# Kernel optimization log

Measured on AMD Instinct MI355X. Metric: run time of the kernel, lower is better.

The kernel has to match this reference:

```python
import jax, jax.numpy as jnp
import numpy as np

NUM_SCOPE = 64
NUM_SAMPLE = 16
DIM_ENCODE = 64


def _fixed_basis(dim):
    # FixedTimeEncoder / FixedFrequencyEncoder basis: w_i = 1 / 10^(9*i/(dim-1))
    return (1.0 / 10.0 ** jnp.linspace(0.0, 9.0, dim)).astype(jnp.float32)


def _cos_encode(t, dim):
    # t: [...] -> [..., dim]
    w = _fixed_basis(dim)
    return jnp.cos(t[..., None] * w)


def setup_inputs() -> dict:
    key = jax.random.key(0)
    ks = jax.random.split(key, 12)
    n, b, df = 4096, NUM_SCOPE, 172
    s_in = 1.0 / np.sqrt(df)
    return {
        "root_node_feature": jax.random.normal(ks[0], (n, df), jnp.float32),
        "root_ts": jax.random.uniform(ks[1], (n,), jnp.float32) * 1e4,
        "neighbor_node_feature": jax.random.normal(ks[2], (n, b, df), jnp.float32),
        "neighbor_edge_feature": jax.random.normal(ks[3], (n, b, df), jnp.float32),
        "neighbor_ts": jax.random.uniform(ks[4], (n, b), jnp.float32) * 1e4,
        "neighbor_nid": jax.random.randint(ks[5], (n, b), 0, 10000, jnp.int64) if jax.config.jax_enable_x64 else jax.random.randint(ks[5], (n, b), 0, 10000, jnp.int32),
        "W_node": jax.random.normal(ks[6], (df, 64), jnp.float32) * s_in,
        "b_node": jnp.zeros((64,), jnp.float32),
        "W_edge": jax.random.normal(ks[7], (df, 64), jnp.float32) * s_in,
        "b_edge": jnp.zeros((64,), jnp.float32),
        "W_link": jax.random.normal(ks[8], (320, 256), jnp.float32) / np.sqrt(320),
        "W_root": jax.random.normal(ks[9], (192, 256), jnp.float32) / np.sqrt(192),
    }


def reference(root_node_feature, root_ts, neighbor_node_feature,
              neighbor_edge_feature, neighbor_ts, neighbor_nid,
              W_node, b_node, W_edge, b_edge, W_link, W_root):
    n, b = neighbor_nid.shape
    # --- encode root node ---
    root_feat = jax.nn.relu(root_node_feature @ W_node + b_node)          # [n,64]
    root_time = _cos_encode(jnp.zeros((n,), jnp.float32), DIM_ENCODE)     # [n,64]
    root_freq = _cos_encode(jnp.ones((n,), jnp.float32), DIM_ENCODE)      # [n,64]
    root_encode = jnp.concatenate([root_feat, root_time, root_freq], 1)   # [n,192]
    # --- encode links ---
    node_enc = jax.nn.relu(neighbor_node_feature @ W_node + b_node)       # [n,b,64]
    edge_enc = jax.nn.relu(neighbor_edge_feature @ W_edge + b_edge)       # [n,b,64]
    neigh_time = root_ts[:, None] - neighbor_ts                           # [n,b]
    time_enc = _cos_encode(neigh_time, DIM_ENCODE)                        # [n,b,64]
    # pairwise equality mask + frequency count (keep_dummy_freq=True)
    neigh_mask = (neighbor_nid[:, :, None] == neighbor_nid[:, None, :])   # [n,b,b]
    neigh_freq = neigh_mask.sum(-1).astype(jnp.float32) / NUM_SCOPE       # [n,b]
    freq_enc = _cos_encode(neigh_freq, DIM_ENCODE)                        # [n,b,64]
    iden_enc = neigh_mask.astype(jnp.float32)                             # [n,b,b]
    link_encode = jnp.concatenate(
        [node_enc, edge_enc, time_enc, freq_enc, iden_enc], axis=-1)      # [n,b,320]
    # --- link mapper: project links & root, score, softmax over neighbors ---
    h_link = jax.nn.relu(jnp.einsum('nbd,dh->nbh', link_encode, W_link))  # [n,b,256]
    h_root = jax.nn.relu(root_encode @ W_root)                            # [n,256]
    scores = jnp.einsum('nbh,nh->nb', h_link, h_root) / jnp.sqrt(256.0)
    probs = jax.nn.softmax(scores, axis=-1)                               # [n,b]
    # --- weighted sampling WITHOUT replacement via Gumbel top-k ---
    g = jax.random.gumbel(jax.random.key(42), (n, b), jnp.float32)
    logp = jnp.log(probs + 1e-20)
    _, action = jax.lax.top_k(logp + g, NUM_SAMPLE)                       # [n,num_sample]
    return probs, action
```

## Files before the change

kernel.cpp:

```cpp
#include <hip/hip_runtime.h>
#include <cstdint>
#include <math.h>

#define B       64
#define DF      172
#define HDIM    256
#define KSAMP   16
#define THREADS 512

typedef const __attribute__((address_space(1))) unsigned int* gp_t;
typedef __attribute__((address_space(3))) unsigned int* lp_t;

#define FMA4(A_, S_, W_) \
  A_.x = fmaf(S_, W_.x, A_.x); A_.y = fmaf(S_, W_.y, A_.y); \
  A_.z = fmaf(S_, W_.z, A_.z); A_.w = fmaf(S_, W_.w, A_.w);

__device__ __forceinline__ uint32_t rotl32(uint32_t x, int d) {
  return (x << d) | (x >> (32 - d));
}

__device__ __forceinline__ void threefry2x32(uint32_t k0, uint32_t k1,
                                             uint32_t& x0, uint32_t& x1) {
  const uint32_t ks0 = k0, ks1 = k1, ks2 = k0 ^ k1 ^ 0x1BD11BDAu;
  x0 += ks0; x1 += ks1;
#define TF_R4(ra,rb,rc,rd) \
  x0 += x1; x1 = rotl32(x1, ra); x1 ^= x0; \
  x0 += x1; x1 = rotl32(x1, rb); x1 ^= x0; \
  x0 += x1; x1 = rotl32(x1, rc); x1 ^= x0; \
  x0 += x1; x1 = rotl32(x1, rd); x1 ^= x0;
  TF_R4(13,15,26,6)  x0 += ks1; x1 += ks2 + 1u;
  TF_R4(17,29,16,24) x0 += ks2; x1 += ks0 + 2u;
  TF_R4(13,15,26,6)  x0 += ks0; x1 += ks1 + 3u;
  TF_R4(17,29,16,24) x0 += ks1; x1 += ks2 + 4u;
  TF_R4(13,15,26,6)  x0 += ks2; x1 += ks0 + 5u;
#undef TF_R4
}

__device__ __forceinline__ void stage_async(const float* __restrict__ g,
                                            float* l, int t) {
#pragma unroll
  for (int it = 0; it < 5; ++it) {
    const int i  = it * 512 + t;
    const int ib = it * 512 + (t & ~63);
    __builtin_amdgcn_global_load_lds((gp_t)(g + i * 4), (lp_t)(l + ib * 4), 16, 0, 0);
  }
  if (t < 192) {
    const int i  = 2560 + t;
    const int ib = 2560 + (t & ~63);
    __builtin_amdgcn_global_load_lds((gp_t)(g + i * 4), (lp_t)(l + ib * 4), 16, 0, 0);
  }
}

#define ENC_STEP(W0_, W1_, W2_, W3_, KK_) { \
  const float4 x0 = A0[(KK_) >> 2]; \
  const float4 x1 = A1[(KK_) >> 2]; \
  FMA4(acc0, x0.x, W0_) FMA4(acc0, x0.y, W1_) FMA4(acc0, x0.z, W2_) FMA4(acc0, x0.w, W3_) \
  FMA4(acc1, x1.x, W0_) FMA4(acc1, x1.y, W1_) FMA4(acc1, x1.z, W2_) FMA4(acc1, x1.w, W3_) }

#define ENC_LOAD(W0_, W1_, W2_, W3_, KK_) { \
  W0_ = W4[(KK_) * 16 + cg]; W1_ = W4[((KK_) + 1) * 16 + cg]; \
  W2_ = W4[((KK_) + 2) * 16 + cg]; W3_ = W4[((KK_) + 3) * 16 + cg]; }

__device__ __forceinline__ void enc_gemm_ring(const float* __restrict__ stage,
                                              const float* __restrict__ W,
                                              const float* __restrict__ bias,
                                              float* __restrict__ out,
                                              int b2, int cg) {
  const float4* W4 = (const float4*)W;
  const float4* A0 = (const float4*)(stage + (2 * b2) * DF);
  const float4* A1 = (const float4*)(stage + (2 * b2 + 1) * DF);
  float4 acc0 = ((const float4*)bias)[cg];
  float4 acc1 = acc0;
  float4 a0, a1, a2, a3, b0, b1, b2_, b3, c0, c1, c2, c3;
  ENC_LOAD(a0, a1, a2, a3, 0)
  ENC_LOAD(b0, b1, b2_, b3, 4)
  ENC_LOAD(c0, c1, c2, c3, 8)
  for (int k0 = 0; k0 < 156; k0 += 12) {
    ENC_STEP(a0, a1, a2, a3, k0)       ENC_LOAD(a0, a1, a2, a3, k0 + 12)
    ENC_STEP(b0, b1, b2_, b3, k0 + 4)  ENC_LOAD(b0, b1, b2_, b3, k0 + 16)
    ENC_STEP(c0, c1, c2, c3, k0 + 8)   ENC_LOAD(c0, c1, c2, c3, k0 + 20)
  }
  ENC_STEP(a0, a1, a2, a3, 156)  ENC_LOAD(a0, a1, a2, a3, 168)
  ENC_STEP(b0, b1, b2_, b3, 160)
  ENC_STEP(c0, c1, c2, c3, 164)
  ENC_STEP(a0, a1, a2, a3, 168)
  float4 o0 = make_float4(fmaxf(acc0.x, 0.f), fmaxf(acc0.y, 0.f), fmaxf(acc0.z, 0.f), fmaxf(acc0.w, 0.f));
  float4 o1 = make_float4(fmaxf(acc1.x, 0.f), fmaxf(acc1.y, 0.f), fmaxf(acc1.z, 0.f), fmaxf(acc1.w, 0.f));
  ((float4*)out)[(2 * b2) * 16 + cg]     = o0;
  ((float4*)out)[(2 * b2 + 1) * 16 + cg] = o1;
}

__device__ __forceinline__ void enc_gemm_lite(const float* __restrict__ stage,
                                              const float* __restrict__ W,
                                              const float* __restrict__ bias,
                                              float* __restrict__ out,
                                              int b2, int cg) {
  const float4* W4 = (const float4*)W;
  const float4* A0 = (const float4*)(stage + (2 * b2) * DF);
  const float4* A1 = (const float4*)(stage + (2 * b2 + 1) * DF);
  float4 acc0 = ((const float4*)bias)[cg];
  float4 acc1 = acc0;
  float4 w0 = W4[0 * 16 + cg], w1 = W4[1 * 16 + cg];
  float4 w2 = W4[2 * 16 + cg], w3 = W4[3 * 16 + cg];
  for (int k = 0; k < DF; k += 4) {
    const float4 wa = w0, wb = w1, wc = w2, wd = w3;
    if (k < DF - 4) {
      w0 = W4[(k + 4) * 16 + cg]; w1 = W4[(k + 5) * 16 + cg];
      w2 = W4[(k + 6) * 16 + cg]; w3 = W4[(k + 7) * 16 + cg];
    }
    ENC_STEP(wa, wb, wc, wd, k)
  }
  float4 o0 = make_float4(fmaxf(acc0.x, 0.f), fmaxf(acc0.y, 0.f), fmaxf(acc0.z, 0.f), fmaxf(acc0.w, 0.f));
  float4 o1 = make_float4(fmaxf(acc1.x, 0.f), fmaxf(acc1.y, 0.f), fmaxf(acc1.z, 0.f), fmaxf(acc1.w, 0.f));
  ((float4*)out)[(2 * b2) * 16 + cg]     = o0;
  ((float4*)out)[(2 * b2 + 1) * 16 + cg] = o1;
}

__device__ __forceinline__ void accum16(float2 (&acc)[16],
                                        const float* __restrict__ enc, int r16,
                                        const float2* __restrict__ Wlp) {
  float2 w0 = Wlp[0], w1 = Wlp[128], w2 = Wlp[256], w3 = Wlp[384];
  for (int d0 = 0; d0 < 64; d0 += 4) {
    const float2 wa = w0, wb = w1, wc = w2, wd = w3;
    if (d0 < 60) {
      const float2* p = Wlp + (d0 + 4) * 128;
      w0 = p[0]; w1 = p[128]; w2 = p[256]; w3 = p[384];
    }
#pragma unroll
    for (int i = 0; i < 16; ++i) {
      const float4 e = *(const float4*)&enc[(r16 + i) * 64 + d0];
      acc[i].x = fmaf(e.x, wa.x, acc[i].x); acc[i].y = fmaf(e.x, wa.y, acc[i].y);
      acc[i].x = fmaf(e.y, wb.x, acc[i].x); acc[i].y = fmaf(e.y, wb.y, acc[i].y);
      acc[i].x = fmaf(e.z, wc.x, acc[i].x); acc[i].y = fmaf(e.z, wc.y, acc[i].y);
      acc[i].x = fmaf(e.w, wd.x, acc[i].x); acc[i].y = fmaf(e.w, wd.y, acc[i].y);
    }
  }
}

__global__ __launch_bounds__(THREADS, 4)
void AdaptSampler_kernel(const float* __restrict__ rootf,
                         const float* __restrict__ root_ts,
                         const float* __restrict__ nf,
                         const float* __restrict__ ef,
                         const float* __restrict__ nts,
                         const int*   __restrict__ nid,
                         const float* __restrict__ Wn,
                         const float* __restrict__ bn,
                         const float* __restrict__ We,
                         const float* __restrict__ be,
                         const float* __restrict__ Wl,
                         const float* __restrict__ Wr,
                         float* __restrict__ out_probs,
                         float* __restrict__ out_action)
{
  __shared__ float nf_stage[B * DF];
  __shared__ float encA[B * 64];
  __shared__ float encB[B * 64];
  __shared__ float hroot_lds[HDIM];
  __shared__ float rootenc_lds[192];
  __shared__ float w_lds[B];
  __shared__ float ts_lds[B];
  __shared__ __align__(16) int nid_lds[B];
  __shared__ float freq_lds[B];
  __shared__ unsigned long long mask_lds[B];
  __shared__ float scpart[4][16][2];

  const int n = blockIdx.x;
  const int t = threadIdx.x;
  const int c2  = t & 127;
  const int r16 = (t >> 7) * 16;
  const int b2 = t >> 4;
  const int cg = t & 15;
  const float2* Wl2 = (const float2*)Wl;

  stage_async(nf + (size_t)n * B * DF, nf_stage, t);
  if (t >= 448) {
    const int j = t - 448;
    double e = 9.0 * (double)j / 63.0;
    const float wj = (float)(1.0 / pow(10.0, e));
    w_lds[j]   = wj;
    nid_lds[j] = nid[n * B + j];
    ts_lds[j]  = nts[n * B + j];
    float a = bn[j];
    const float* rr = rootf + (size_t)n * DF;
#pragma unroll 4
    for (int d = 0; d < DF; ++d) a = fmaf(rr[d], Wn[d * 64 + j], a);
    rootenc_lds[j]       = fmaxf(a, 0.0f);
    rootenc_lds[64 + j]  = 1.0f;
    rootenc_lds[128 + j] = cosf(wj);
    const int my = nid_lds[j];
    unsigned long long m = 0ull;
    for (int k = 0; k < B; ++k)
      m |= ((unsigned long long)(nid_lds[k] == my)) << k;
    mask_lds[j] = m;
    freq_lds[j] = (float)__popcll(m) * 0.015625f;
  }
  __syncthreads();

  enc_gemm_ring(nf_stage, Wn, bn, encA, b2, cg);
  {
    const float rts = root_ts[n];
#pragma unroll
    for (int q = 0; q < 8; ++q) {
      const int idx = q * 512 + t;
      const int bb = idx >> 6, dd = idx & 63;
      encB[idx] = cosf((rts - ts_lds[bb]) * w_lds[dd]);
    }
  }
  {
    const int h = t >> 1, hf = t & 1;
    float a = 0.0f;
    for (int d = hf * 96; d < hf * 96 + 96; ++d)
      a = fmaf(rootenc_lds[d], Wr[d * HDIM + h], a);
    a += __shfl_xor(a, 1);
    if (hf == 0) hroot_lds[h] = fmaxf(a, 0.0f);
  }
  __syncthreads();

  stage_async(ef + (size_t)n * B * DF, nf_stage, t);
  float2 acc[16];
#pragma unroll
  for (int i = 0; i < 16; ++i) acc[i] = make_float2(0.f, 0.f);
  accum16(acc, encA, r16, Wl2 + c2);
  __syncthreads();

  enc_gemm_lite(nf_stage, We, be, encA, b2, cg);
  __syncthreads();

#pragma unroll
  for (int q = 0; q < 8; ++q) {
    const int idx = q * 512 + t;
    const int bb = idx >> 6, dd = idx & 63;
    nf_stage[idx] = cosf(freq_lds[bb] * w_lds[dd]);
  }
  accum16(acc, encA, r16, Wl2 + 64 * 128 + c2);
  __syncthreads();

  accum16(acc, encB, r16, Wl2 + 128 * 128 + c2);
  accum16(acc, nf_stage, r16, Wl2 + 192 * 128 + c2);
  {
    const float2* Wlp = Wl2 + 256 * 128 + c2;
#pragma unroll
    for (int i = 0; i < 16; ++i) {
      unsigned long long m = mask_lds[r16 + i];
      while (m) {
        const int d = __builtin_ctzll(m);
        m &= m - 1;
        const float2 wv = Wlp[d * 128];
        acc[i].x += wv.x;
        acc[i].y += wv.y;
      }
    }
  }

  {
    const float2 hr = ((const float2*)hroot_lds)[c2];
#pragma unroll
    for (int i = 0; i < 16; ++i) {
      float s = fmaxf(acc[i].x, 0.f) * hr.x;
      s = fmaf(fmaxf(acc[i].y, 0.f), hr.y, s);
#pragma unroll
      for (int mm = 32; mm >= 1; mm >>= 1) s += __shfl_xor(s, mm);
      if ((t & 63) == 0) scpart[t >> 7][i][(t >> 6) & 1] = s;
    }
  }
  __syncthreads();

  if (t < B) {
    float s = (scpart[t >> 4][t & 15][0] + scpart[t >> 4][t & 15][1]) * 0.0625f;
    float m = s;
#pragma unroll
    for (int mm = 32; mm >= 1; mm >>= 1) m = fmaxf(m, __shfl_xor(m, mm));
    float e = expf(s - m);
    float sum = e;
#pragma unroll
    for (int mm = 32; mm >= 1; mm >>= 1) sum += __shfl_xor(sum, mm);
    float p = e / sum;
    out_probs[(size_t)n * B + t] = p;

    uint32_t i = (uint32_t)(n * B + t);
    uint32_t x0 = 0u, x1 = i;
    threefry2x32(0u, 42u, x0, x1);
    uint32_t bits = x0 ^ x1;
    float f = __uint_as_float((bits >> 9) | 0x3f800000u) - 1.0f;
    const float TINY = 1.1754943508222875e-38f;
    float u = fmaxf(f * (1.0f - TINY) + TINY, TINY);
    float g = -logf(-logf(u));
    float keyv = logf(p + 1e-20f) + g;

    float v = keyv;
    for (int k = 0; k < KSAMP; ++k) {
      float bv = v; int bi = t;
#pragma unroll
      for (int mm = 32; mm >= 1; mm >>= 1) {
        float ov = __shfl_xor(bv, mm);
        int   oi = __shfl_xor(bi, mm);
        if (ov > bv || (ov == bv && oi < bi)) { bv = ov; bi = oi; }
      }
      if (t == 0) out_action[(size_t)n * KSAMP + k] = (float)bi;
      if (t == bi) v = -3.402823466e+38f;
    }
  }
}

extern "C" void kernel_launch(void* const* d_in, const int* in_sizes, int n_in,
                              void* d_out, int out_size, void* d_ws, size_t ws_size,
                              hipStream_t stream) {
  const float* rootf = (const float*)d_in[0];
  const float* rts   = (const float*)d_in[1];
  const float* nf    = (const float*)d_in[2];
  const float* ef    = (const float*)d_in[3];
  const float* nts   = (const float*)d_in[4];
  const int*   nid   = (const int*)d_in[5];
  const float* Wn    = (const float*)d_in[6];
  const float* bn    = (const float*)d_in[7];
  const float* We    = (const float*)d_in[8];
  const float* be    = (const float*)d_in[9];
  const float* Wl    = (const float*)d_in[10];
  const float* Wr    = (const float*)d_in[11];

  const int n = in_sizes[1];
  float* probs  = (float*)d_out;
  float* action = probs + (size_t)n * B;

  AdaptSampler_kernel<<<dim3(n), dim3(THREADS), 0, stream>>>(
      rootf, rts, nf, ef, nts, nid, Wn, bn, We, be, Wl, Wr, probs, action);
}
```

Baseline: 879.3 us.

## Split each row's neighbors across two blocks and move softmax/top-k to second kernel

The fused per-row kernel is split in two. The first runs a 2D grid where each 256-thread block handles half of a row's 64 neighbors (32 each) and writes raw scores. A second small kernel then does the softmax, Gumbel noise and top-k per row. This halves per-block LDS so more blocks can be resident and parallelism rises. The cost is a second launch, a global round-trip for the scores, and duplicated root-encoding and h_root work in both half-blocks.

```diff
diff --git a/kernel.cpp b/kernel.cpp
--- a/kernel.cpp
+++ b/kernel.cpp
@@ -3,10 +3,11 @@
 #include <math.h>
 
 #define B       64
+#define RH      32
 #define DF      172
 #define HDIM    256
 #define KSAMP   16
-#define THREADS 512
+#define T1      256
 
 typedef const __attribute__((address_space(1))) unsigned int* gp_t;
 typedef __attribute__((address_space(3))) unsigned int* lp_t;
@@ -36,17 +37,17 @@
 #undef TF_R4
 }
 
-__device__ __forceinline__ void stage_async(const float* __restrict__ g,
-                                            float* l, int t) {
+__device__ __forceinline__ void stage32(const float* __restrict__ g,
+                                        float* l, int t) {
 #pragma unroll
   for (int it = 0; it < 5; ++it) {
-    const int i  = it * 512 + t;
-    const int ib = it * 512 + (t & ~63);
+    const int i  = it * 256 + t;
+    const int ib = it * 256 + (t & ~63);
     __builtin_amdgcn_global_load_lds((gp_t)(g + i * 4), (lp_t)(l + ib * 4), 16, 0, 0);
   }
-  if (t < 192) {
-    const int i  = 2560 + t;
-    const int ib = 2560 + (t & ~63);
+  if (t < 96) {
+    const int i  = 1280 + t;
+    const int ib = 1280 + (t & ~63);
     __builtin_amdgcn_global_load_lds((gp_t)(g + i * 4), (lp_t)(l + ib * 4), 16, 0, 0);
   }
 }
@@ -137,50 +138,49 @@
   }
 }
 
-__global__ __launch_bounds__(THREADS, 4)
-void AdaptSampler_kernel(const float* __restrict__ rootf,
-                         const float* __restrict__ root_ts,
-                         const float* __restrict__ nf,
-                         const float* __restrict__ ef,
-                         const float* __restrict__ nts,
-                         const int*   __restrict__ nid,
-                         const float* __restrict__ Wn,
-                         const float* __restrict__ bn,
-                         const float* __restrict__ We,
-                         const float* __restrict__ be,
-                         const float* __restrict__ Wl,
-                         const float* __restrict__ Wr,
-                         float* __restrict__ out_probs,
-                         float* __restrict__ out_action)
+__global__ __launch_bounds__(T1, 4)
+void enc_score_kernel(const float* __restrict__ rootf,
+                      const float* __restrict__ root_ts,
+                      const float* __restrict__ nf,
+                      const float* __restrict__ ef,
+                      const float* __restrict__ nts,
+                      const int*   __restrict__ nid,
+                      const float* __restrict__ Wn, const float* __restrict__ bn,
+                      const float* __restrict__ We, const float* __restrict__ be,
+                      const float* __restrict__ Wl,
+                      const float* __restrict__ Wr,
+                      float* __restrict__ out_sc)
 {
-  __shared__ float nf_stage[B * DF];
-  __shared__ float encA[B * 64];
-  __shared__ float encB[B * 64];
+  __shared__ float stage[RH * DF];
+  __shared__ float encA[RH * 64];
+  __shared__ float encB[RH * 64];
   __shared__ float hroot_lds[HDIM];
   __shared__ float rootenc_lds[192];
   __shared__ float w_lds[B];
-  __shared__ float ts_lds[B];
-  __shared__ __align__(16) int nid_lds[B];
-  __shared__ float freq_lds[B];
-  __shared__ unsigned long long mask_lds[B];
-  __shared__ float scpart[4][16][2];
-
-  const int n = blockIdx.x;
-  const int t = threadIdx.x;
+  __shared__ float ts_lds[RH];
+  __shared__ int   nid_lds[B];
+  __shared__ float freq_lds[RH];
+  __shared__ unsigned long long mask_lds[RH];
+  __shared__ float scpart[2][16][2];
+
+  const int n  = blockIdx.x;
+  const int hb = blockIdx.y;
+  const int r0 = hb * RH;
+  const int t  = threadIdx.x;
   const int c2  = t & 127;
   const int r16 = (t >> 7) * 16;
   const int b2 = t >> 4;
   const int cg = t & 15;
   const float2* Wl2 = (const float2*)Wl;
 
-  stage_async(nf + (size_t)n * B * DF, nf_stage, t);
-  if (t >= 448) {
-    const int j = t - 448;
+  stage32(nf + (size_t)n * B * DF + (size_t)r0 * DF, stage, t);
+  if (t >= 192) {
+    const int j = t - 192;
     double e = 9.0 * (double)j / 63.0;
     const float wj = (float)(1.0 / pow(10.0, e));
     w_lds[j]   = wj;
     nid_lds[j] = nid[n * B + j];
-    ts_lds[j]  = nts[n * B + j];
+    if (j < RH) ts_lds[j] = nts[n * B + r0 + j];
     float a = bn[j];
     const float* rr = rootf + (size_t)n * DF;
 #pragma unroll 4
@@ -188,56 +188,58 @@
     rootenc_lds[j]       = fmaxf(a, 0.0f);
     rootenc_lds[64 + j]  = 1.0f;
     rootenc_lds[128 + j] = cosf(wj);
-    const int my = nid_lds[j];
-    unsigned long long m = 0ull;
-    for (int k = 0; k < B; ++k)
-      m |= ((unsigned long long)(nid_lds[k] == my)) << k;
-    mask_lds[j] = m;
-    freq_lds[j] = (float)__popcll(m) * 0.015625f;
-  }
-  __syncthreads();
-
-  enc_gemm_ring(nf_stage, Wn, bn, encA, b2, cg);
+    if (j < RH) {
+      const int my = nid_lds[r0 + j];
+      unsigned long long m = 0ull;
+      for (int k = 0; k < B; ++k)
+        m |= ((unsigned long long)(nid_lds[k] == my)) << k;
+      mask_lds[j] = m;
+      freq_lds[j] = (float)__popcll(m) * 0.015625f;
+    }
+  }
+  __syncthreads();
+
+  enc_gemm_ring(stage, Wn, bn, encA, b2, cg);
   {
     const float rts = root_ts[n];
 #pragma unroll
     for (int q = 0; q < 8; ++q) {
-      const int idx = q * 512 + t;
+      const int idx = q * 256 + t;
       const int bb = idx >> 6, dd = idx & 63;
       encB[idx] = cosf((rts - ts_lds[bb]) * w_lds[dd]);
     }
   }
   {
-    const int h = t >> 1, hf = t & 1;
-    float a = 0.0f;
-    for (int d = hf * 96; d < hf * 96 + 96; ++d)
-      a = fmaf(rootenc_lds[d], Wr[d * HDIM + h], a);
-    a += __shfl_xor(a, 1);
-    if (hf == 0) hroot_lds[h] = fmaxf(a, 0.0f);
-  }
-  __syncthreads();
-
-  stage_async(ef + (size_t)n * B * DF, nf_stage, t);
+    float a0 = 0.0f, a1 = 0.0f;
+#pragma unroll 4
+    for (int d = 0; d < 96; ++d)   a0 = fmaf(rootenc_lds[d], Wr[d * HDIM + t], a0);
+#pragma unroll 4
+    for (int d = 96; d < 192; ++d) a1 = fmaf(rootenc_lds[d], Wr[d * HDIM + t], a1);
+    hroot_lds[t] = fmaxf(a0 + a1, 0.0f);
+  }
+  __syncthreads();
+
+  stage32(ef + (size_t)n * B * DF + (size_t)r0 * DF, stage, t);
   float2 acc[16];
 #pragma unroll
   for (int i = 0; i < 16; ++i) acc[i] = make_float2(0.f, 0.f);
   accum16(acc, encA, r16, Wl2 + c2);
   __syncthreads();
 
-  enc_gemm_lite(nf_stage, We, be, encA, b2, cg);
+  enc_gemm_lite(stage, We, be, encA, b2, cg);
   __syncthreads();
 
 #pragma unroll
   for (int q = 0; q < 8; ++q) {
-    const int idx = q * 512 + t;
+    const int idx = q * 256 + t;
     const int bb = idx >> 6, dd = idx & 63;
-    nf_stage[idx] = cosf(freq_lds[bb] * w_lds[dd]);
+    stage[idx] = cosf(freq_lds[bb] * w_lds[dd]);
   }
   accum16(acc, encA, r16, Wl2 + 64 * 128 + c2);
   __syncthreads();
 
   accum16(acc, encB, r16, Wl2 + 128 * 128 + c2);
-  accum16(acc, nf_stage, r16, Wl2 + 192 * 128 + c2);
+  accum16(acc, stage, r16, Wl2 + 192 * 128 + c2);
   {
     const float2* Wlp = Wl2 + 256 * 128 + c2;
 #pragma unroll
@@ -266,40 +268,50 @@
   }
   __syncthreads();
 
-  if (t < B) {
-    float s = (scpart[t >> 4][t & 15][0] + scpart[t >> 4][t & 15][1]) * 0.0625f;
-    float m = s;
-#pragma unroll
-    for (int mm = 32; mm >= 1; mm >>= 1) m = fmaxf(m, __shfl_xor(m, mm));
-    float e = expf(s - m);
-    float sum = e;
-#pragma unroll
-    for (int mm = 32; mm >= 1; mm >>= 1) sum += __shfl_xor(sum, mm);
-    float p = e / sum;
-    out_probs[(size_t)n * B + t] = p;
-
-    uint32_t i = (uint32_t)(n * B + t);
-    uint32_t x0 = 0u, x1 = i;
-    threefry2x32(0u, 42u, x0, x1);
-    uint32_t bits = x0 ^ x1;
-    float f = __uint_as_float((bits >> 9) | 0x3f800000u) - 1.0f;
-    const float TINY = 1.1754943508222875e-38f;
-    float u = fmaxf(f * (1.0f - TINY) + TINY, TINY);
-    float g = -logf(-logf(u));
-    float keyv = logf(p + 1e-20f) + g;
-
-    float v = keyv;
-    for (int k = 0; k < KSAMP; ++k) {
-      float bv = v; int bi = t;
-#pragma unroll
-      for (int mm = 32; mm >= 1; mm >>= 1) {
-        float ov = __shfl_xor(bv, mm);
-        int   oi = __shfl_xor(bi, mm);
-        if (ov > bv || (ov == bv && oi < bi)) { bv = ov; bi = oi; }
-      }
-      if (t == 0) out_action[(size_t)n * KSAMP + k] = (float)bi;
-      if (t == bi) v = -3.402823466e+38f;
-    }
+  if (t < RH) {
+    const float s = scpart[t >> 4][t & 15][0] + scpart[t >> 4][t & 15][1];
+    out_sc[(size_t)n * B + r0 + t] = s;
+  }
+}
+
+__global__ __launch_bounds__(64, 8)
+void softmax_topk_kernel(float* __restrict__ probs,
+                         float* __restrict__ out_action)
+{
+  const int n = blockIdx.x;
+  const int t = threadIdx.x;
+  float s = probs[(size_t)n * B + t] * 0.0625f;
+  float m = s;
+#pragma unroll
+  for (int mm = 32; mm >= 1; mm >>= 1) m = fmaxf(m, __shfl_xor(m, mm));
+  float e = expf(s - m);
+  float sum = e;
+#pragma unroll
+  for (int mm = 32; mm >= 1; mm >>= 1) sum += __shfl_xor(sum, mm);
+  float p = e / sum;
+  probs[(size_t)n * B + t] = p;
+
+  uint32_t i = (uint32_t)(n * B + t);
+  uint32_t x0 = 0u, x1 = i;
+  threefry2x32(0u, 42u, x0, x1);
+  uint32_t bits = x0 ^ x1;
+  float f = __uint_as_float((bits >> 9) | 0x3f800000u) - 1.0f;
+  const float TINY = 1.1754943508222875e-38f;
+  float u = fmaxf(f * (1.0f - TINY) + TINY, TINY);
+  float g = -logf(-logf(u));
+  float keyv = logf(p + 1e-20f) + g;
+
+  float v = keyv;
+  for (int k = 0; k < KSAMP; ++k) {
+    float bv = v; int bi = t;
+#pragma unroll
+    for (int mm = 32; mm >= 1; mm >>= 1) {
+      float ov = __shfl_xor(bv, mm);
+      int   oi = __shfl_xor(bi, mm);
+      if (ov > bv || (ov == bv && oi < bi)) { bv = ov; bi = oi; }
+    }
+    if (t == 0) out_action[(size_t)n * KSAMP + k] = (float)bi;
+    if (t == bi) v = -3.402823466e+38f;
   }
 }
 
@@ -323,6 +335,7 @@
   float* probs  = (float*)d_out;
   float* action = probs + (size_t)n * B;
 
-  AdaptSampler_kernel<<<dim3(n), dim3(THREADS), 0, stream>>>(
-      rootf, rts, nf, ef, nts, nid, Wn, bn, We, be, Wl, Wr, probs, action);
-}
+  enc_score_kernel<<<dim3(n, 2), dim3(T1), 0, stream>>>(
+      rootf, rts, nf, ef, nts, nid, Wn, bn, We, be, Wl, Wr, probs);
+  softmax_topk_kernel<<<dim3(n), dim3(64), 0, stream>>>(probs, action);
+}
```

After: 896.0 us. No clear change (+1.9%).
